# Performance work log

Measured on AMD Instinct MI355X. Metric: run time of the kernel, lower is better.

The kernel has to match this reference:

```python
import jax, jax.numpy as jnp
import numpy as np

B_SZ = 64
SEQ = 2048
IN_DIM = 16
D_MODEL = 128
D_INNER = 256   # expand(2) * d_model
D_STATE = 16
N_LAYERS = 5
N_PARAMS = 3
IDX_PRICE, IDX_RY, IDX_GY, IDX_NY = 0, 1, 2, 3


def setup_inputs() -> dict:
    key = jax.random.key(0)
    ks = iter(jax.random.split(key, 64))
    def nrm(shape, scale=0.02):
        return jax.random.normal(next(ks), shape, jnp.float32) * scale
    inp = {}
    # forward args
    inp["origins"] = jax.random.uniform(next(ks), (B_SZ, SEQ, IN_DIM), jnp.float32, 0.5, 1.5)
    inp["x"] = jax.random.normal(next(ks), (B_SZ, SEQ, IN_DIM), jnp.float32)
    # input embedding
    inp["emb_w"] = nrm((IN_DIM, D_MODEL)); inp["emb_b"] = jnp.zeros((D_MODEL,), jnp.float32)
    # per-layer Mamba block params, stacked on leading n_layers dim
    inp["in_w"] = nrm((N_LAYERS, D_MODEL, 2 * D_INNER)); inp["in_b"] = jnp.zeros((N_LAYERS, 2 * D_INNER), jnp.float32)
    inp["xp_w"] = nrm((N_LAYERS, D_INNER, 2 * D_STATE)); inp["xp_b"] = jnp.zeros((N_LAYERS, 2 * D_STATE), jnp.float32)
    inp["dt_w"] = nrm((N_LAYERS, D_INNER, D_INNER));     inp["dt_b"] = jnp.zeros((N_LAYERS, D_INNER), jnp.float32)
    inp["out_w"] = nrm((N_LAYERS, D_INNER, D_MODEL));    inp["out_b"] = jnp.zeros((N_LAYERS, D_MODEL), jnp.float32)
    # A_log init: log(arange(1, d_state+1)) broadcast over d_inner
    a = jnp.log(jnp.arange(1, D_STATE + 1, dtype=jnp.float32))
    inp["A_log"] = jnp.broadcast_to(a, (N_LAYERS, D_INNER, D_STATE)).copy()
    inp["Dp"] = jnp.ones((N_LAYERS, D_INNER), jnp.float32)
    # layernorms
    inp["ln_g"] = jnp.ones((N_LAYERS, D_MODEL), jnp.float32)
    inp["ln_b"] = jnp.zeros((N_LAYERS, D_MODEL), jnp.float32)
    # output head: Linear(128,64) -> ReLU -> Linear(64,3) -> Sigmoid
    inp["o1_w"] = nrm((D_MODEL, D_MODEL // 2)); inp["o1_b"] = jnp.zeros((D_MODEL // 2,), jnp.float32)
    inp["o2_w"] = nrm((D_MODEL // 2, N_PARAMS)); inp["o2_b"] = jnp.zeros((N_PARAMS,), jnp.float32)
    return inp


def _silu(x):
    return x * jax.nn.sigmoid(x)


def _layernorm(x, g, b, eps=1e-5):
    mu = jnp.mean(x, axis=-1, keepdims=True)
    var = jnp.mean(jnp.square(x - mu), axis=-1, keepdims=True)
    return (x - mu) * jax.lax.rsqrt(var + eps) * g + b


def _mamba_block(x, iw, ib, xw, xb, dw, db, ow, ob, alog, d):
    # x: [B, S, D_MODEL]
    xz = x @ iw + ib                       # [B,S,2*di]
    x_proj, z = jnp.split(xz, 2, axis=-1)  # [B,S,di] each
    u = _silu(x_proj)                      # no conv path (use_conv=False)
    A = -jnp.exp(alog)                     # [di, ds]
    x_dbl = u @ xw + xb                    # [B,S,2*ds]
    Bm, Cm = jnp.split(x_dbl, 2, axis=-1)  # [B,S,ds]
    dt = jax.nn.softplus(u @ dw + db)      # [B,S,di]

    def step(h, t):
        u_t, dt_t, B_t, C_t = t            # [B,di],[B,di],[B,ds],[B,ds]
        dA = jnp.exp(dt_t[:, :, None] * A)                 # [B,di,ds]
        h = h * dA + (dt_t * u_t)[:, :, None] * B_t[:, None, :]
        y = jnp.sum(h * C_t[:, None, :], axis=-1) + d * u_t  # [B,di]
        return h, y

    h0 = jnp.zeros((u.shape[0], u.shape[2], A.shape[-1]), u.dtype)
    xs = (jnp.swapaxes(u, 0, 1), jnp.swapaxes(dt, 0, 1),
          jnp.swapaxes(Bm, 0, 1), jnp.swapaxes(Cm, 0, 1))  # seq-major
    _, ys = jax.lax.scan(step, h0, xs)     # ys: [S,B,di]
    y = jnp.swapaxes(ys, 0, 1)             # [B,S,di]
    y = y * _silu(z)
    return y @ ow + ob                     # [B,S,D_MODEL]


def _forward(origins, x, emb_w, emb_b, in_w, in_b, xp_w, xp_b, dt_w, dt_b,
             out_w, out_b, A_log, Dp, ln_g, ln_b, o1_w, o1_b, o2_w, o2_b):
    h = x @ emb_w + emb_b
    for l in range(N_LAYERS):
        res = h
        h = _mamba_block(h, in_w[l], in_b[l], xp_w[l], xp_b[l], dt_w[l], dt_b[l],
                         out_w[l], out_b[l], A_log[l], Dp[l])
        h = _layernorm(h + res, ln_g[l], ln_b[l])
    pooled = jnp.mean(h, axis=1)                         # lengths=None path
    hid = jax.nn.relu(pooled @ o1_w + o1_b)              # dropout is eval no-op
    params = jax.nn.sigmoid(hid @ o2_w + o2_b) * 2.0     # [B, 3]
    a, b, c = params[:, 0], params[:, 1], params[:, 2]
    last_1 = origins[:, -1, :]
    last_2 = origins[:, -2, :]
    price = last_1[:, IDX_PRICE]
    ry_now, ry_before = last_1[:, IDX_RY], last_2[:, IDX_RY]
    gy_now, gy_before = last_1[:, IDX_GY], last_2[:, IDX_GY]
    ny_now, ny_before = last_1[:, IDX_NY], last_2[:, IDX_NY]
    out = price * a * ry_now / ry_before * 2.0 * (
        b * jax.nn.sigmoid(gy_now - gy_before) + c * jax.nn.sigmoid(ny_now - ny_before))
    return out  # [B]


def reference(origins, x, emb_w, emb_b, in_w, in_b, xp_w, xp_b, dt_w, dt_b,
              out_w, out_b, A_log, Dp, ln_g, ln_b, o1_w, o1_b, o2_w, o2_b):
    return _forward(origins, x, emb_w, emb_b, in_w, in_b, xp_w, xp_b, dt_w, dt_b,
                    out_w, out_b, A_log, Dp, ln_g, ln_b, o1_w, o1_b, o2_w, o2_b)
```

## Files before the change

### kernel.cpp

```cpp
#include <hip/hip_runtime.h>
#include <hip/hip_bf16.h>
#include <math.h>

#define B_SZ    64
#define SEQ     2048
#define DMODEL  128
#define DINNER  256
#define DSTATE  16
#define NLAYERS 5
#define NSEG    32
#define LSEG    64

typedef unsigned short u16;
typedef __attribute__((ext_vector_type(8))) short bf16x8;
typedef __attribute__((ext_vector_type(4))) float f32x4;

static __device__ __forceinline__ float bf2f(u16 u){
  union { unsigned u; float f; } a; a.u = ((unsigned)u) << 16; return a.f;
}
static __device__ __forceinline__ u16 f2bf(float f){
  union { float f; unsigned u; } a; a.f = f;
  unsigned r = a.u + 0x7fffu + ((a.u >> 16) & 1u);
  return (u16)(r >> 16);
}
static __device__ __forceinline__ float sigm(float x){ return 1.f/(1.f+__expf(-x)); }
static __device__ __forceinline__ float siluf(float x){ return x/(1.f+__expf(-x)); }

#define MFMA16(a,b,c) __builtin_amdgcn_mfma_f32_16x16x32_bf16((a),(b),(c),0,0,0)

__global__ __launch_bounds__(256) void prep_kernel(
    const float* __restrict__ in_w, const float* __restrict__ xp_w,
    const float* __restrict__ dt_w, const float* __restrict__ out_w,
    u16* __restrict__ WT1, u16* __restrict__ WT2, u16* __restrict__ WT3){
  int idx = blockIdx.x*256 + threadIdx.x;
  const int n1 = NLAYERS*512*128, n2 = NLAYERS*288*256, n3 = NLAYERS*128*256;
  if (idx < n1){
    int l = idx/(512*128), r = idx%(512*128), n = r/128, k = r%128;
    WT1[idx] = f2bf(in_w[((size_t)l*128 + k)*512 + n]);
  } else if (idx < n1+n2){
    int t = idx-n1; int l=t/(288*256), r=t%(288*256), n=r/256, k=r%256;
    float v = (n<32) ? xp_w[((size_t)l*256+k)*32 + n]
                     : dt_w[((size_t)l*256+k)*256 + (n-32)];
    WT2[t] = f2bf(v);
  } else if (idx < n1+n2+n3){
    int t = idx-n1-n2; int l=t/(128*256), r=t%(128*256), n=r/256, k=r%256;
    WT3[t] = f2bf(out_w[((size_t)l*256+k)*128 + n]);
  }
}

__global__ __launch_bounds__(256) void emb_kernel(
    const float* __restrict__ x, const float* __restrict__ ew,
    const float* __restrict__ eb, u16* __restrict__ Hb, size_t cs){
  int idx = blockIdx.x*256 + threadIdx.x;
  int m = idx >> 7, d = idx & 127;
  float s = eb[d];
  #pragma unroll
  for (int k=0;k<16;++k) s += x[(size_t)m*16+k]*ew[k*128+d];
  Hb[(size_t)(d>>4)*cs + (size_t)m*16 + (d&15)] = f2bf(s);
}

__global__ __launch_bounds__(256) void gemm1_kernel(
    const u16* __restrict__ Hb, const u16* __restrict__ WT,
    const float* __restrict__ bias, u16* __restrict__ U, u16* __restrict__ ZS,
    size_t cs){
  const int lane = threadIdx.x & 63, wave = threadIdx.x >> 6;
  const int half = blockIdx.x & 1;
  const int m0 = (blockIdx.x >> 1)*256 + wave*64;
  const int lr = lane & 15, kg = lane >> 4;
  bf16x8 hfrag[4][4];
  #pragma unroll
  for (int g=0; g<4; ++g)
    #pragma unroll
    for (int f=0; f<4; ++f)
      hfrag[g][f] = *(const bf16x8*)(Hb + (size_t)((kg>>1)+2*f)*cs
                                     + (size_t)(m0+g*16+lr)*16 + (kg&1)*8);
  u16* const dst = half ? ZS : U;
  const u16* wrow = WT + (size_t)(half*256+lr)*128 + kg*8;
  bf16x8 wv[4];
  #pragma unroll
  for (int f=0; f<4; ++f) wv[f] = *(const bf16x8*)(wrow + f*32);
  #pragma unroll
  for (int nn=0; nn<16; ++nn){
    bf16x8 wn[4];
    if (nn < 15){
      const u16* wr2 = wrow + (size_t)(nn+1)*16*128;
      #pragma unroll
      for (int f=0; f<4; ++f) wn[f] = *(const bf16x8*)(wr2 + f*32);
    }
    f32x4 acc[4];
    #pragma unroll
    for (int g=0; g<4; ++g){
      acc[g] = (f32x4){0.f,0.f,0.f,0.f};
      #pragma unroll
      for (int f=0; f<4; ++f) acc[g] = MFMA16(wv[f], hfrag[g][f], acc[g]);
    }
    float4 bs4 = *(const float4*)(bias + half*256 + nn*16 + kg*4);
    #pragma unroll
    for (int g=0; g<4; ++g){
      ushort4 uv;
      uv.x = f2bf(siluf(acc[g][0]+bs4.x));
      uv.y = f2bf(siluf(acc[g][1]+bs4.y));
      uv.z = f2bf(siluf(acc[g][2]+bs4.z));
      uv.w = f2bf(siluf(acc[g][3]+bs4.w));
      *(ushort4*)(dst + (size_t)nn*cs + (size_t)(m0+g*16+lr)*16 + kg*4) = uv;
    }
    #pragma unroll
    for (int f=0; f<4; ++f) wv[f] = wn[f];
  }
}

__global__ __launch_bounds__(256) void gemm2_kernel(
    const u16* __restrict__ Uin, const u16* __restrict__ WT,
    const float* __restrict__ xpb, const float* __restrict__ dtb,
    float* __restrict__ BCf, u16* __restrict__ DT, size_t cs){
  const int lane = threadIdx.x & 63, wave = threadIdx.x >> 6;
  const int m0 = blockIdx.x*128 + wave*32;
  const int lr = lane & 15, kg = lane >> 4;
  bf16x8 hfrag[2][8];
  #pragma unroll
  for (int g=0; g<2; ++g)
    #pragma unroll
    for (int f=0; f<8; ++f)
      hfrag[g][f] = *(const bf16x8*)(Uin + (size_t)((kg>>1)+2*f)*cs
                                     + (size_t)(m0+g*16+lr)*16 + (kg&1)*8);
  const u16* wrow = WT + (size_t)lr*256 + kg*8;
  bf16x8 wv[8];
  #pragma unroll
  for (int f=0; f<8; ++f) wv[f] = *(const bf16x8*)(wrow + f*32);
  #pragma unroll
  for (int nn=0; nn<18; ++nn){
    bf16x8 wn[8];
    if (nn < 17){
      const u16* wr2 = wrow + (size_t)(nn+1)*16*256;
      #pragma unroll
      for (int f=0; f<8; ++f) wn[f] = *(const bf16x8*)(wr2 + f*32);
    }
    f32x4 acc[2];
    #pragma unroll
    for (int g=0; g<2; ++g){
      acc[g] = (f32x4){0.f,0.f,0.f,0.f};
      #pragma unroll
      for (int f=0; f<8; ++f) acc[g] = MFMA16(wv[f], hfrag[g][f], acc[g]);
    }
    const int col0 = nn*16 + kg*4;
    if (col0 < 32){
      float4 bs4 = *(const float4*)(xpb + col0);
      #pragma unroll
      for (int g=0; g<2; ++g){
        float4 ov;
        ov.x = acc[g][0]+bs4.x; ov.y = acc[g][1]+bs4.y;
        ov.z = acc[g][2]+bs4.z; ov.w = acc[g][3]+bs4.w;
        *(float4*)(BCf + (size_t)nn*cs + (size_t)(m0+g*16+lr)*16 + kg*4) = ov;
      }
    } else {
      float4 bs4 = *(const float4*)(dtb + (col0-32));
      #pragma unroll
      for (int g=0; g<2; ++g){
        float v0=acc[g][0]+bs4.x, v1=acc[g][1]+bs4.y;
        float v2=acc[g][2]+bs4.z, v3=acc[g][3]+bs4.w;
        ushort4 uv;
        uv.x = f2bf(fmaxf(v0,0.f) + __logf(1.f + __expf(-fabsf(v0))));
        uv.y = f2bf(fmaxf(v1,0.f) + __logf(1.f + __expf(-fabsf(v1))));
        uv.z = f2bf(fmaxf(v2,0.f) + __logf(1.f + __expf(-fabsf(v2))));
        uv.w = f2bf(fmaxf(v3,0.f) + __logf(1.f + __expf(-fabsf(v3))));
        *(ushort4*)(DT + (size_t)(nn-2)*cs + (size_t)(m0+g*16+lr)*16 + kg*4) = uv;
      }
    }
    #pragma unroll
    for (int f=0; f<8; ++f) wv[f] = wn[f];
  }
}

static __device__ __forceinline__ void powtree(float r, float* pw){
  float p2=r*r, p3=p2*r, p4=p2*p2;
  float p5=p4*r, p6=p4*p2, p7=p4*p3, p8=p4*p4;
  pw[0]=r;  pw[1]=p2; pw[2]=p3; pw[3]=p4;
  pw[4]=p5; pw[5]=p6; pw[6]=p7; pw[7]=p8;
  pw[8]=p8*r;  pw[9]=p8*p2;  pw[10]=p8*p3;  pw[11]=p8*p4;
  pw[12]=p8*p5; pw[13]=p8*p6; pw[14]=p8*p7; pw[15]=p8*p8;
}

__global__ __launch_bounds__(256) void scan_p1(
    const u16* __restrict__ U, const u16* __restrict__ DT,
    const float* __restrict__ BCf, const float* __restrict__ Alog,
    u16* __restrict__ SGH, float* __restrict__ SDT, size_t cs){
  const int seg = blockIdx.x % NSEG;
  const int b   = blockIdx.x / NSEG;
  const int c   = threadIdx.x;
  const size_t coff = (size_t)(c>>4)*cs + (c&15);
  float a2[16]; bool geo = true;
  #pragma unroll
  for (int i=0;i<16;++i){
    float A = -__expf(Alog[c*16+i]);
    a2[i] = A * 1.44269504f;
    if (fabsf(A + (float)(i+1)) > 1e-3f) geo = false;
  }
  float h[16];
  #pragma unroll
  for (int i=0;i<16;++i) h[i]=0.f;
  float sdt = 0.f;
  const size_t mbase = (size_t)b*SEQ + (size_t)seg*LSEG;
  if (geo){
    #pragma unroll 2
    for (int t=0;t<LSEG;++t){
      const size_t m = mbase + t;
      float u  = bf2f(U [coff + m*16]);
      float dt = bf2f(DT[coff + m*16]);
      const float* bp = BCf + m*16;
      float du = dt*u; sdt += dt;
      float r = exp2f(-1.44269504f*dt);
      float pw[16]; powtree(r, pw);
      #pragma unroll
      for (int i=0;i<16;++i) h[i] = h[i]*pw[i] + du*bp[i];
    }
  } else {
    for (int t=0;t<LSEG;++t){
      const size_t m = mbase + t;
      float u  = bf2f(U [coff + m*16]);
      float dt = bf2f(DT[coff + m*16]);
      const float* bp = BCf + m*16;
      float du = dt*u; sdt += dt;
      #pragma unroll
      for (int i=0;i<16;++i)
        h[i] = h[i]*exp2f(dt*a2[i]) + du*bp[i];
    }
  }
  const size_t kb = ((size_t)b*NSEG+seg);
  #pragma unroll
  for (int i=0;i<16;++i) SGH[(kb*16+i)*256 + c] = f2bf(h[i]);
  SDT[kb*256 + c] = sdt;
}

__global__ __launch_bounds__(256) void scan_p2(
    u16* __restrict__ SGH, const float* __restrict__ SDT,
    const float* __restrict__ Alog){
  const int i = blockIdx.x & 15, b = blockIdx.x >> 4, c = threadIdx.x;
  const float a2 = -__expf(Alog[c*16+i]) * 1.44269504f;
  float h = 0.f;
  for (int s=0;s<NSEG;++s){
    const size_t kb = ((size_t)b*NSEG+s);
    float sdt = SDT[kb*256 + c];
    size_t k = (kb*16+i)*256 + c;
    float hl = bf2f(SGH[k]);
    SGH[k] = f2bf(h);
    h = h*exp2f(sdt*a2) + hl;
  }
}

__global__ __launch_bounds__(256) void scan_p3(
    u16* __restrict__ UY, const u16* __restrict__ DT, const float* __restrict__ BCf,
    const u16* __restrict__ ZS, const float* __restrict__ Alog,
    const float* __restrict__ Dp, const u16* __restrict__ SGH, size_t cs){
  const int seg = blockIdx.x % NSEG;
  const int b   = blockIdx.x / NSEG;
  const int c   = threadIdx.x;
  const size_t coff = (size_t)(c>>4)*cs + (c&15);
  float a2[16]; bool geo = true;
  #pragma unroll
  for (int i=0;i<16;++i){
    float A = -__expf(Alog[c*16+i]);
    a2[i] = A * 1.44269504f;
    if (fabsf(A + (float)(i+1)) > 1e-3f) geo = false;
  }
  const float Dv = Dp[c];
  const size_t kb = ((size_t)b*NSEG+seg);
  float h[16];
  #pragma unroll
  for (int i=0;i<16;++i) h[i] = bf2f(SGH[(kb*16+i)*256 + c]);
  const size_t mbase = (size_t)b*SEQ + (size_t)seg*LSEG;
  if (geo){
    #pragma unroll 2
    for (int t=0;t<LSEG;++t){
      const size_t m = mbase + t;
      float u  = bf2f(UY[coff + m*16]);
      float dt = bf2f(DT[coff + m*16]);
      float zs = bf2f(ZS[coff + m*16]);
      const float* bp = BCf + m*16;
      const float* cp = BCf + cs + m*16;
      float du = dt*u;
      float r = exp2f(-1.44269504f*dt);
      float pw[16]; powtree(r, pw);
      float s0=0.f, s1=0.f;
      #pragma unroll
      for (int i=0;i<8;++i){
        h[i] = h[i]*pw[i] + du*bp[i];
        s0 += h[i]*cp[i];
      }
      #pragma unroll
      for (int i=8;i<16;++i){
        h[i] = h[i]*pw[i] + du*bp[i];
        s1 += h[i]*cp[i];
      }
      float y = s0 + s1 + Dv*u;
      UY[coff + m*16] = f2bf(y*zs);
    }
  } else {
    for (int t=0;t<LSEG;++t){
      const size_t m = mbase + t;
      float u  = bf2f(UY[coff + m*16]);
      float dt = bf2f(DT[coff + m*16]);
      float zs = bf2f(ZS[coff + m*16]);
      const float* bp = BCf + m*16;
      const float* cp = BCf + cs + m*16;
      float du = dt*u;
      float s0=0.f, s1=0.f;
      #pragma unroll
      for (int i=0;i<16;++i){
        h[i] = h[i]*exp2f(dt*a2[i]) + du*bp[i];
        s0 += h[i]*cp[i];
      }
      float y = s0 + s1 + Dv*u;
      UY[coff + m*16] = f2bf(y*zs);
    }
  }
}

__global__ __launch_bounds__(256) void gemm3ln_kernel(
    const u16* __restrict__ YS, const u16* __restrict__ WT,
    const float* __restrict__ ob, const float* __restrict__ g,
    const float* __restrict__ bb, u16* __restrict__ Hb, size_t cs){
  const int lane = threadIdx.x & 63, wave = threadIdx.x >> 6;
  const int m0 = blockIdx.x*128 + wave*32;
  const int lr = lane & 15, kg = lane >> 4;
  bf16x8 hfrag[2][8];
  #pragma unroll
  for (int gg=0; gg<2; ++gg)
    #pragma unroll
    for (int f=0; f<8; ++f)
      hfrag[gg][f] = *(const bf16x8*)(YS + (size_t)((kg>>1)+2*f)*cs
                                      + (size_t)(m0+gg*16+lr)*16 + (kg&1)*8);
  const u16* wrow = WT + (size_t)lr*256 + kg*8;
  bf16x8 wv[8];
  #pragma unroll
  for (int f=0; f<8; ++f) wv[f] = *(const bf16x8*)(wrow + f*32);
  ushort4 xvp[2][8];
  float s[2] = {0.f,0.f}, q[2] = {0.f,0.f};
  #pragma unroll
  for (int n=0; n<8; ++n){
    bf16x8 wn[8];
    if (n < 7){
      const u16* wr2 = wrow + (size_t)(n+1)*16*256;
      #pragma unroll
      for (int f=0; f<8; ++f) wn[f] = *(const bf16x8*)(wr2 + f*32);
    }
    float4 bs4 = *(const float4*)(ob + n*16 + kg*4);
    #pragma unroll
    for (int gg=0; gg<2; ++gg){
      f32x4 acc = {0.f,0.f,0.f,0.f};
      #pragma unroll
      for (int f=0; f<8; ++f) acc = MFMA16(wv[f], hfrag[gg][f], acc);
      const size_t m = (size_t)(m0 + gg*16 + lr);
      ushort4 rs = *(const ushort4*)(Hb + (size_t)n*cs + m*16 + kg*4);
      float x0 = acc[0] + bs4.x + bf2f(rs.x);
      float x1 = acc[1] + bs4.y + bf2f(rs.y);
      float x2 = acc[2] + bs4.z + bf2f(rs.z);
      float x3 = acc[3] + bs4.w + bf2f(rs.w);
      s[gg] += (x0+x1)+(x2+x3);
      q[gg] += (x0*x0+x1*x1)+(x2*x2+x3*x3);
      ushort4 pv; pv.x=f2bf(x0); pv.y=f2bf(x1); pv.z=f2bf(x2); pv.w=f2bf(x3);
      xvp[gg][n] = pv;
    }
    #pragma unroll
    for (int f=0; f<8; ++f) wv[f] = wn[f];
  }
  #pragma unroll
  for (int gg=0; gg<2; ++gg){
    float ss = s[gg], qq = q[gg];
    ss += __shfl_xor(ss,16); qq += __shfl_xor(qq,16);
    ss += __shfl_xor(ss,32); qq += __shfl_xor(qq,32);
    float mu  = ss * 0.0078125f;
    float var = qq * 0.0078125f - mu*mu;
    float inv = rsqrtf(var + 1e-5f);
    const size_t m = (size_t)(m0 + gg*16 + lr);
    #pragma unroll
    for (int n=0;n<8;++n){
      float4 g4 = *(const float4*)(g  + n*16 + kg*4);
      float4 b4 = *(const float4*)(bb + n*16 + kg*4);
      ushort4 pv = xvp[gg][n];
      ushort4 uv;
      uv.x = f2bf((bf2f(pv.x)-mu)*inv*g4.x + b4.x);
      uv.y = f2bf((bf2f(pv.y)-mu)*inv*g4.y + b4.y);
      uv.z = f2bf((bf2f(pv.z)-mu)*inv*g4.z + b4.z);
      uv.w = f2bf((bf2f(pv.w)-mu)*inv*g4.w + b4.w);
      *(ushort4*)(Hb + (size_t)n*cs + m*16 + kg*4) = uv;
    }
  }
}

__global__ __launch_bounds__(128) void pool1_kernel(
    const u16* __restrict__ Hb, float* __restrict__ PP, size_t cs){
  const int blk = blockIdx.x;
  const int tc = blk & 15, b = blk >> 4;
  const int d = threadIdx.x;
  const size_t coff = (size_t)(d>>4)*cs + (d&15);
  float s = 0.f;
  const size_t base = ((size_t)b*SEQ + tc*128);
  for (int t=0;t<128;++t) s += bf2f(Hb[coff + (base+t)*16]);
  PP[((size_t)b*16 + tc)*128 + d] = s;
}
__global__ __launch_bounds__(128) void pool2_kernel(
    const float* __restrict__ PP, float* __restrict__ P){
  const int b = blockIdx.x, d = threadIdx.x;
  float s = 0.f;
  #pragma unroll
  for (int tc=0;tc<16;++tc) s += PP[((size_t)b*16+tc)*128 + d];
  P[b*128 + d] = s * (1.f/SEQ);
}

__global__ __launch_bounds__(64) void head_kernel(
    const float* __restrict__ P, const float* __restrict__ o1w,
    const float* __restrict__ o1b, const float* __restrict__ o2w,
    const float* __restrict__ o2b, const float* __restrict__ origins,
    float* __restrict__ out){
  const int b = blockIdx.x;
  const int j = threadIdx.x;
  float hv = o1b[j];
  #pragma unroll 4
  for (int d=0; d<128; ++d) hv += P[b*128+d]*o1w[d*64+j];
  hv = fmaxf(hv, 0.f);
  float p0 = hv*o2w[j*3+0], p1 = hv*o2w[j*3+1], p2 = hv*o2w[j*3+2];
  #pragma unroll
  for (int o=1;o<64;o<<=1){
    p0 += __shfl_xor(p0,o); p1 += __shfl_xor(p1,o); p2 += __shfl_xor(p2,o);
  }
  if (j == 0){
    float a = 2.f*sigm(p0 + o2b[0]);
    float bb = 2.f*sigm(p1 + o2b[1]);
    float c = 2.f*sigm(p2 + o2b[2]);
    const float* l1 = origins + ((size_t)b*SEQ + (SEQ-1))*16;
    const float* l2 = origins + ((size_t)b*SEQ + (SEQ-2))*16;
    float price=l1[0], ry_n=l1[1], ry_b=l2[1], gy_n=l1[2], gy_b=l2[2], ny_n=l1[3], ny_b=l2[3];
    out[b] = price*a*ry_n/ry_b*2.f*(bb*sigm(gy_n-gy_b) + c*sigm(ny_n-ny_b));
  }
}

extern "C" void kernel_launch(void* const* d_in, const int* in_sizes, int n_in,
                              void* d_out, int out_size, void* d_ws, size_t ws_size,
                              hipStream_t stream){
  const float* origins = (const float*)d_in[0];
  const float* x      = (const float*)d_in[1];
  const float* emb_w  = (const float*)d_in[2];
  const float* emb_b  = (const float*)d_in[3];
  const float* in_w   = (const float*)d_in[4];
  const float* in_b   = (const float*)d_in[5];
  const float* xp_w   = (const float*)d_in[6];
  const float* xp_b   = (const float*)d_in[7];
  const float* dt_w   = (const float*)d_in[8];
  const float* dt_b   = (const float*)d_in[9];
  const float* out_w  = (const float*)d_in[10];
  const float* out_b  = (const float*)d_in[11];
  const float* A_log  = (const float*)d_in[12];
  const float* Dp     = (const float*)d_in[13];
  const float* ln_g   = (const float*)d_in[14];
  const float* ln_b   = (const float*)d_in[15];
  const float* o1_w   = (const float*)d_in[16];
  const float* o1_b   = (const float*)d_in[17];
  const float* o2_w   = (const float*)d_in[18];
  const float* o2_b   = (const float*)d_in[19];
  float* outp = (float*)d_out;

  auto al = [](size_t b)->size_t{ return (b + 255) & ~(size_t)255; };
  const size_t wt1_b = al((size_t)NLAYERS*512*128*2);
  const size_t wt2_b = al((size_t)NLAYERS*288*256*2);
  const size_t wt3_b = al((size_t)NLAYERS*128*256*2);
  const size_t po_b  = al((size_t)B_SZ*128*4);
  const size_t pp_b  = al((size_t)B_SZ*16*128*4);
  const size_t fixed = wt1_b + wt2_b + wt3_b + po_b + pp_b;

  int CB = 0;
  static const int cbc[7] = {64,32,16,8,4,2,1};
  size_t hb_b=0, u_b=0, bc_b=0, sgh_b=0, sdt_b=0;
  for (int i=0;i<7;++i){
    int cb = cbc[i];
    size_t csz = (size_t)cb*SEQ*16;
    size_t hbb = al(8*csz*2);
    size_t uu  = al(16*csz*2);
    size_t bb  = al(2*csz*4);
    size_t sgh = al((size_t)cb*NSEG*DSTATE*DINNER*2);
    size_t sdt = al((size_t)cb*NSEG*DINNER*4);
    if (fixed + hbb + 3*uu + bb + sgh + sdt <= ws_size){
      CB=cb; hb_b=hbb; u_b=uu; bc_b=bb; sgh_b=sgh; sdt_b=sdt; break;
    }
  }
  if (!CB) return;

  char* ws = (char*)d_ws;
  size_t off = 0;
  auto take = [&](size_t bytes)->char*{ char* p = ws + off; off += bytes; return p; };
  u16*   WT1 = (u16*)take(wt1_b);
  u16*   WT2 = (u16*)take(wt2_b);
  u16*   WT3 = (u16*)take(wt3_b);
  float* PO  = (float*)take(po_b);
  float* PP  = (float*)take(pp_b);
  u16*   Hb  = (u16*)take(hb_b);
  u16*   U   = (u16*)take(u_b);
  u16*   ZS  = (u16*)take(u_b);
  u16*   DT  = (u16*)take(u_b);
  float* BCf = (float*)take(bc_b);
  u16*   SGH = (u16*)take(sgh_b);
  float* SDT = (float*)take(sdt_b);

  prep_kernel<<<3360, 256, 0, stream>>>(in_w, xp_w, dt_w, out_w, WT1, WT2, WT3);

  const int NC = B_SZ / CB;
  const int Mc = CB * SEQ;
  const size_t cs = (size_t)Mc*16;
  for (int ci=0; ci<NC; ++ci){
    const int b0 = ci * CB;
    const size_t R0 = (size_t)b0 * SEQ;
    emb_kernel<<<(Mc*DMODEL)/256, 256, 0, stream>>>(x + R0*16, emb_w, emb_b, Hb, cs);
    for (int l=0;l<NLAYERS;++l){
      const float* Al = A_log + (size_t)l*DINNER*DSTATE;
      gemm1_kernel<<<(Mc/256)*2, 256, 0, stream>>>(Hb, WT1 + (size_t)l*512*128,
                                                   in_b + l*512, U, ZS, cs);
      gemm2_kernel<<<Mc/128, 256, 0, stream>>>(U, WT2 + (size_t)l*288*256,
                                               xp_b + l*32, dt_b + l*256, BCf, DT, cs);
      scan_p1<<<CB*NSEG, 256, 0, stream>>>(U, DT, BCf, Al, SGH, SDT, cs);
      scan_p2<<<CB*16, 256, 0, stream>>>(SGH, SDT, Al);
      scan_p3<<<CB*NSEG, 256, 0, stream>>>(U, DT, BCf, ZS, Al, Dp + l*DINNER,
                                           SGH, cs);
      gemm3ln_kernel<<<Mc/128, 256, 0, stream>>>(U, WT3 + (size_t)l*128*256,
                                                 out_b + l*128, ln_g + l*128,
                                                 ln_b + l*128, Hb, cs);
    }
    pool1_kernel<<<CB*16, 128, 0, stream>>>(Hb, PP, cs);
    pool2_kernel<<<CB, 128, 0, stream>>>(PP, PO + (size_t)b0*128);
  }
  head_kernel<<<B_SZ, 64, 0, stream>>>(PO, o1_w, o1_b, o2_w, o2_b, origins, outp);
}
```

Before: 1.885 ms.

## Pack scan state with dt sums and pick batch chunking by workspace

The per-segment dt sum now lives inside the SGH buffer as an extra bf16 row, and the PP pooling buffer shares memory with SGH. The chunk-size search also considers fewer scan segments and bf16 storage for the B/C projections. Together these shrink the workspace so larger batch chunks can fit, which means fewer kernel launches and more parallelism per launch. The costs are storing the dt sum in bf16 and, on the fallback paths, bf16 B/C, both of which lose precision.

```diff
diff --git a/kernel.cpp b/kernel.cpp
--- a/kernel.cpp
+++ b/kernel.cpp
@@ -8,8 +8,6 @@
 #define DINNER  256
 #define DSTATE  16
 #define NLAYERS 5
-#define NSEG    32
-#define LSEG    64
 
 typedef unsigned short u16;
 typedef __attribute__((ext_vector_type(8))) short bf16x8;
@@ -109,10 +107,11 @@
   }
 }
 
+template<int BF>
 __global__ __launch_bounds__(256) void gemm2_kernel(
     const u16* __restrict__ Uin, const u16* __restrict__ WT,
     const float* __restrict__ xpb, const float* __restrict__ dtb,
-    float* __restrict__ BCf, u16* __restrict__ DT, size_t cs){
+    void* __restrict__ BCv, u16* __restrict__ DT, size_t cs){
   const int lane = threadIdx.x & 63, wave = threadIdx.x >> 6;
   const int m0 = blockIdx.x*128 + wave*32;
   const int lr = lane & 15, kg = lane >> 4;
@@ -147,10 +146,17 @@
       float4 bs4 = *(const float4*)(xpb + col0);
       #pragma unroll
       for (int g=0; g<2; ++g){
-        float4 ov;
-        ov.x = acc[g][0]+bs4.x; ov.y = acc[g][1]+bs4.y;
-        ov.z = acc[g][2]+bs4.z; ov.w = acc[g][3]+bs4.w;
-        *(float4*)(BCf + (size_t)nn*cs + (size_t)(m0+g*16+lr)*16 + kg*4) = ov;
+        if (BF){
+          float4 ov;
+          ov.x = acc[g][0]+bs4.x; ov.y = acc[g][1]+bs4.y;
+          ov.z = acc[g][2]+bs4.z; ov.w = acc[g][3]+bs4.w;
+          *(float4*)((float*)BCv + (size_t)nn*cs + (size_t)(m0+g*16+lr)*16 + kg*4) = ov;
+        } else {
+          ushort4 uv;
+          uv.x = f2bf(acc[g][0]+bs4.x); uv.y = f2bf(acc[g][1]+bs4.y);
+          uv.z = f2bf(acc[g][2]+bs4.z); uv.w = f2bf(acc[g][3]+bs4.w);
+          *(ushort4*)((u16*)BCv + (size_t)nn*cs + (size_t)(m0+g*16+lr)*16 + kg*4) = uv;
+        }
       }
     } else {
       float4 bs4 = *(const float4*)(dtb + (col0-32));
@@ -180,12 +186,14 @@
   pw[12]=p8*p5; pw[13]=p8*p6; pw[14]=p8*p7; pw[15]=p8*p8;
 }
 
+
+template<int BF>
 __global__ __launch_bounds__(256) void scan_p1(
     const u16* __restrict__ U, const u16* __restrict__ DT,
-    const float* __restrict__ BCf, const float* __restrict__ Alog,
-    u16* __restrict__ SGH, float* __restrict__ SDT, size_t cs){
-  const int seg = blockIdx.x % NSEG;
-  const int b   = blockIdx.x / NSEG;
+    const void* __restrict__ BCv, const float* __restrict__ Alog,
+    u16* __restrict__ SGH, size_t cs, int nseg, int L){
+  const int seg = blockIdx.x % nseg;
+  const int b   = blockIdx.x / nseg;
   const int c   = threadIdx.x;
   const size_t coff = (size_t)(c>>4)*cs + (c&15);
   float a2[16]; bool geo = true;
@@ -199,60 +207,81 @@
   #pragma unroll
   for (int i=0;i<16;++i) h[i]=0.f;
   float sdt = 0.f;
-  const size_t mbase = (size_t)b*SEQ + (size_t)seg*LSEG;
+  const size_t mbase = (size_t)b*SEQ + (size_t)seg*L;
   if (geo){
     #pragma unroll 2
-    for (int t=0;t<LSEG;++t){
+    for (int t=0;t<L;++t){
       const size_t m = mbase + t;
       float u  = bf2f(U [coff + m*16]);
       float dt = bf2f(DT[coff + m*16]);
-      const float* bp = BCf + m*16;
+      float Bv[16];
+      if (BF){
+        const float* bp = (const float*)BCv + m*16;
+        #pragma unroll
+        for (int i=0;i<16;++i) Bv[i] = bp[i];
+      } else {
+        bf16x8 b0 = *(const bf16x8*)((const u16*)BCv + m*16);
+        bf16x8 b1 = *(const bf16x8*)((const u16*)BCv + m*16 + 8);
+        #pragma unroll
+        for (int i=0;i<8;++i){ Bv[i]=bf2f((u16)b0[i]); Bv[i+8]=bf2f((u16)b1[i]); }
+      }
       float du = dt*u; sdt += dt;
       float r = exp2f(-1.44269504f*dt);
       float pw[16]; powtree(r, pw);
       #pragma unroll
-      for (int i=0;i<16;++i) h[i] = h[i]*pw[i] + du*bp[i];
+      for (int i=0;i<16;++i) h[i] = h[i]*pw[i] + du*Bv[i];
     }
   } else {
-    for (int t=0;t<LSEG;++t){
+    for (int t=0;t<L;++t){
       const size_t m = mbase + t;
       float u  = bf2f(U [coff + m*16]);
       float dt = bf2f(DT[coff + m*16]);
-      const float* bp = BCf + m*16;
+      float Bv[16];
+      if (BF){
+        const float* bp = (const float*)BCv + m*16;
+        #pragma unroll
+        for (int i=0;i<16;++i) Bv[i] = bp[i];
+      } else {
+        bf16x8 b0 = *(const bf16x8*)((const u16*)BCv + m*16);
+        bf16x8 b1 = *(const bf16x8*)((const u16*)BCv + m*16 + 8);
+        #pragma unroll
+        for (int i=0;i<8;++i){ Bv[i]=bf2f((u16)b0[i]); Bv[i+8]=bf2f((u16)b1[i]); }
+      }
       float du = dt*u; sdt += dt;
       #pragma unroll
       for (int i=0;i<16;++i)
-        h[i] = h[i]*exp2f(dt*a2[i]) + du*bp[i];
-    }
-  }
-  const size_t kb = ((size_t)b*NSEG+seg);
-  #pragma unroll
-  for (int i=0;i<16;++i) SGH[(kb*16+i)*256 + c] = f2bf(h[i]);
-  SDT[kb*256 + c] = sdt;
+        h[i] = h[i]*exp2f(dt*a2[i]) + du*Bv[i];
+    }
+  }
+  const size_t kb = ((size_t)b*nseg+seg);
+  #pragma unroll
+  for (int i=0;i<16;++i) SGH[(kb*17+i)*256 + c] = f2bf(h[i]);
+  SGH[(kb*17+16)*256 + c] = f2bf(sdt);
 }
 
 __global__ __launch_bounds__(256) void scan_p2(
-    u16* __restrict__ SGH, const float* __restrict__ SDT,
-    const float* __restrict__ Alog){
+    u16* __restrict__ SGH, const float* __restrict__ Alog, int nseg){
   const int i = blockIdx.x & 15, b = blockIdx.x >> 4, c = threadIdx.x;
   const float a2 = -__expf(Alog[c*16+i]) * 1.44269504f;
   float h = 0.f;
-  for (int s=0;s<NSEG;++s){
-    const size_t kb = ((size_t)b*NSEG+s);
-    float sdt = SDT[kb*256 + c];
-    size_t k = (kb*16+i)*256 + c;
+  for (int s=0;s<nseg;++s){
+    const size_t kb = ((size_t)b*nseg+s);
+    float sdt = bf2f(SGH[(kb*17+16)*256 + c]);
+    size_t k = (kb*17+i)*256 + c;
     float hl = bf2f(SGH[k]);
     SGH[k] = f2bf(h);
     h = h*exp2f(sdt*a2) + hl;
   }
 }
 
+template<int BF>
 __global__ __launch_bounds__(256) void scan_p3(
-    u16* __restrict__ UY, const u16* __restrict__ DT, const float* __restrict__ BCf,
+    u16* __restrict__ UY, const u16* __restrict__ DT, const void* __restrict__ BCv,
     const u16* __restrict__ ZS, const float* __restrict__ Alog,
-    const float* __restrict__ Dp, const u16* __restrict__ SGH, size_t cs){
-  const int seg = blockIdx.x % NSEG;
-  const int b   = blockIdx.x / NSEG;
+    const float* __restrict__ Dp, const u16* __restrict__ SGH, size_t cs,
+    int nseg, int L){
+  const int seg = blockIdx.x % nseg;
+  const int b   = blockIdx.x / nseg;
   const int c   = threadIdx.x;
   const size_t coff = (size_t)(c>>4)*cs + (c&15);
   float a2[16]; bool geo = true;
@@ -263,53 +292,85 @@
     if (fabsf(A + (float)(i+1)) > 1e-3f) geo = false;
   }
   const float Dv = Dp[c];
-  const size_t kb = ((size_t)b*NSEG+seg);
+  const size_t kb = ((size_t)b*nseg+seg);
   float h[16];
   #pragma unroll
-  for (int i=0;i<16;++i) h[i] = bf2f(SGH[(kb*16+i)*256 + c]);
-  const size_t mbase = (size_t)b*SEQ + (size_t)seg*LSEG;
+  for (int i=0;i<16;++i) h[i] = bf2f(SGH[(kb*17+i)*256 + c]);
+  const size_t mbase = (size_t)b*SEQ + (size_t)seg*L;
   if (geo){
     #pragma unroll 2
-    for (int t=0;t<LSEG;++t){
+    for (int t=0;t<L;++t){
       const size_t m = mbase + t;
       float u  = bf2f(UY[coff + m*16]);
       float dt = bf2f(DT[coff + m*16]);
       float zs = bf2f(ZS[coff + m*16]);
-      const float* bp = BCf + m*16;
-      const float* cp = BCf + cs + m*16;
+      float Bv[16], Cv[16];
+      if (BF){
+        const float* bp = (const float*)BCv + m*16;
+        const float* cp = (const float*)BCv + cs + m*16;
+        #pragma unroll
+        for (int i=0;i<16;++i){ Bv[i]=bp[i]; Cv[i]=cp[i]; }
+      } else {
+        const u16* bc = (const u16*)BCv;
+        bf16x8 b0 = *(const bf16x8*)(bc + m*16);
+        bf16x8 b1 = *(const bf16x8*)(bc + m*16 + 8);
+        bf16x8 c0 = *(const bf16x8*)(bc + cs + m*16);
+        bf16x8 c1 = *(const bf16x8*)(bc + cs + m*16 + 8);
+        #pragma unroll
+        for (int i=0;i<8;++i){
+          Bv[i]=bf2f((u16)b0[i]); Bv[i+8]=bf2f((u16)b1[i]);
+          Cv[i]=bf2f((u16)c0[i]); Cv[i+8]=bf2f((u16)c1[i]);
+        }
+      }
       float du = dt*u;
       float r = exp2f(-1.44269504f*dt);
       float pw[16]; powtree(r, pw);
       float s0=0.f, s1=0.f;
       #pragma unroll
       for (int i=0;i<8;++i){
-        h[i] = h[i]*pw[i] + du*bp[i];
-        s0 += h[i]*cp[i];
+        h[i] = h[i]*pw[i] + du*Bv[i];
+        s0 += h[i]*Cv[i];
       }
       #pragma unroll
       for (int i=8;i<16;++i){
-        h[i] = h[i]*pw[i] + du*bp[i];
-        s1 += h[i]*cp[i];
+        h[i] = h[i]*pw[i] + du*Bv[i];
+        s1 += h[i]*Cv[i];
       }
       float y = s0 + s1 + Dv*u;
       UY[coff + m*16] = f2bf(y*zs);
     }
   } else {
-    for (int t=0;t<LSEG;++t){
+    for (int t=0;t<L;++t){
       const size_t m = mbase + t;
       float u  = bf2f(UY[coff + m*16]);
       float dt = bf2f(DT[coff + m*16]);
       float zs = bf2f(ZS[coff + m*16]);
-      const float* bp = BCf + m*16;
-      const float* cp = BCf + cs + m*16;
+      float Bv[16], Cv[16];
+      if (BF){
+        const float* bp = (const float*)BCv + m*16;
+        const float* cp = (const float*)BCv + cs + m*16;
+        #pragma unroll
+        for (int i=0;i<16;++i){ Bv[i]=bp[i]; Cv[i]=cp[i]; }
+      } else {
+        const u16* bc = (const u16*)BCv;
+        bf16x8 b0 = *(const bf16x8*)(bc + m*16);
+        bf16x8 b1 = *(const bf16x8*)(bc + m*16 + 8);
+        bf16x8 c0 = *(const bf16x8*)(bc + cs + m*16);
+        bf16x8 c1 = *(const bf16x8*)(bc + cs + m*16 + 8);
+        #pragma unroll
+        for (int i=0;i<8;++i){
+          Bv[i]=bf2f((u16)b0[i]); Bv[i+8]=bf2f((u16)b1[i]);
+          Cv[i]=bf2f((u16)c0[i]); Cv[i+8]=bf2f((u16)c1[i]);
+        }
+      }
       float du = dt*u;
-      float s0=0.f, s1=0.f;
+      float s0=0.f;
       #pragma unroll
       for (int i=0;i<16;++i){
-        h[i] = h[i]*exp2f(dt*a2[i]) + du*bp[i];
-        s0 += h[i]*cp[i];
-      }
-      float y = s0 + s1 + Dv*u;
+        h[i] = h[i]*exp2f(dt*a2[i]) + du*Bv[i];
+        s0 += h[i]*Cv[i];
+      }
+      float y = s0 + Dv*u;
       UY[coff + m*16] = f2bf(y*zs);
     }
   }
@@ -465,21 +526,26 @@
   const size_t wt3_b = al((size_t)NLAYERS*128*256*2);
   const size_t po_b  = al((size_t)B_SZ*128*4);
   const size_t pp_b  = al((size_t)B_SZ*16*128*4);
-  const size_t fixed = wt1_b + wt2_b + wt3_b + po_b + pp_b;
-
-  int CB = 0;
-  static const int cbc[7] = {64,32,16,8,4,2,1};
-  size_t hb_b=0, u_b=0, bc_b=0, sgh_b=0, sdt_b=0;
-  for (int i=0;i<7;++i){
+  const size_t fixed = wt1_b + wt2_b + wt3_b + po_b;
+
+  int CB = 0, NSEG = 0, BCF = 0;
+  size_t hb_b=0, u_b=0, bc_b=0, sg_b=0;
+  static const int cbc[7]  = {64,32,16,8,4,2,1};
+  static const int nsc[4]  = {32,16,32,16};
+  static const int bfc[4]  = {1,1,0,0};
+  for (int i=0;i<7 && !CB;++i){
     int cb = cbc[i];
     size_t csz = (size_t)cb*SEQ*16;
-    size_t hbb = al(8*csz*2);
-    size_t uu  = al(16*csz*2);
-    size_t bb  = al(2*csz*4);
-    size_t sgh = al((size_t)cb*NSEG*DSTATE*DINNER*2);
-    size_t sdt = al((size_t)cb*NSEG*DINNER*4);
-    if (fixed + hbb + 3*uu + bb + sgh + sdt <= ws_size){
-      CB=cb; hb_b=hbb; u_b=uu; bc_b=bb; sgh_b=sgh; sdt_b=sdt; break;
+    for (int k=0;k<4;++k){
+      int ns = nsc[k], bf = bfc[k];
+      size_t hbb = al(8*csz*2);
+      size_t uu  = al(16*csz*2);
+      size_t bb  = al(2*csz*(bf?4:2));
+      size_t sg  = al((size_t)cb*ns*17*256*2);
+      size_t ov  = (sg > pp_b) ? sg : pp_b;
+      if (fixed + hbb + 3*uu + bb + ov <= ws_size){
+        CB=cb; NSEG=ns; BCF=bf; hb_b=hbb; u_b=uu; bc_b=bb; sg_b=ov; break;
+      }
     }
   }
   if (!CB) return;
@@ -491,19 +557,19 @@
   u16*   WT2 = (u16*)take(wt2_b);
   u16*   WT3 = (u16*)take(wt3_b);
   float* PO  = (float*)take(po_b);
-  float* PP  = (float*)take(pp_b);
   u16*   Hb  = (u16*)take(hb_b);
   u16*   U   = (u16*)take(u_b);
   u16*   ZS  = (u16*)take(u_b);
   u16*   DT  = (u16*)take(u_b);
-  float* BCf = (float*)take(bc_b);
-  u16*   SGH = (u16*)take(sgh_b);
-  float* SDT = (float*)take(sdt_b);
+  void*  BC  = (void*)take(bc_b);
+  u16*   SGH = (u16*)take(sg_b);
+  float* PP  = (float*)SGH;
 
   prep_kernel<<<3360, 256, 0, stream>>>(in_w, xp_w, dt_w, out_w, WT1, WT2, WT3);
 
   const int NC = B_SZ / CB;
   const int Mc = CB * SEQ;
+  const int L  = SEQ / NSEG;
   const size_t cs = (size_t)Mc*16;
   for (int ci=0; ci<NC; ++ci){
     const int b0 = ci * CB;
@@ -513,12 +579,23 @@
       const float* Al = A_log + (size_t)l*DINNER*DSTATE;
       gemm1_kernel<<<(Mc/256)*2, 256, 0, stream>>>(Hb, WT1 + (size_t)l*512*128,
                                                    in_b + l*512, U, ZS, cs);
-      gemm2_kernel<<<Mc/128, 256, 0, stream>>>(U, WT2 + (size_t)l*288*256,
-                                               xp_b + l*32, dt_b + l*256, BCf, DT, cs);
-      scan_p1<<<CB*NSEG, 256, 0, stream>>>(U, DT, BCf, Al, SGH, SDT, cs);
-      scan_p2<<<CB*16, 256, 0, stream>>>(SGH, SDT, Al);
-      scan_p3<<<CB*NSEG, 256, 0, stream>>>(U, DT, BCf, ZS, Al, Dp + l*DINNER,
-                                           SGH, cs);
+      if (BCF)
+        gemm2_kernel<1><<<Mc/128, 256, 0, stream>>>(U, WT2 + (size_t)l*288*256,
+                                                    xp_b + l*32, dt_b + l*256, BC, DT, cs);
+      else
+        gemm2_kernel<0><<<Mc/128, 256, 0, stream>>>(U, WT2 + (size_t)l*288*256,
+                                                    xp_b + l*32, dt_b + l*256, BC, DT, cs);
+      if (BCF){
+        scan_p1<1><<<CB*NSEG, 256, 0, stream>>>(U, DT, BC, Al, SGH, cs, NSEG, L);
+        scan_p2<<<CB*16, 256, 0, stream>>>(SGH, Al, NSEG);
+        scan_p3<1><<<CB*NSEG, 256, 0, stream>>>(U, DT, BC, ZS, Al, Dp + l*DINNER,
+                                                SGH, cs, NSEG, L);
+      } else {
+        scan_p1<0><<<CB*NSEG, 256, 0, stream>>>(U, DT, BC, Al, SGH, cs, NSEG, L);
+        scan_p2<<<CB*16, 256, 0, stream>>>(SGH, Al, NSEG);
+        scan_p3<0><<<CB*NSEG, 256, 0, stream>>>(U, DT, BC, ZS, Al, Dp + l*DINNER,
+                                                SGH, cs, NSEG, L);
+      }
       gemm3ln_kernel<<<Mc/128, 256, 0, stream>>>(U, WT3 + (size_t)l*128*256,
                                                  out_b + l*128, ln_g + l*128,
                                                  ln_b + l*128, Hb, cs);
```

New measurement: 1.832 ms. -2.8%, faster.
